# Optimization experiments

Hardware: AMD Instinct MI355X
Metric: run time of the kernel (lower is better)

Reference implementation:

```python
import jax, jax.numpy as jnp
import numpy as np

K_IN = 9      # input_patch_size
K_OUT = 3     # output_patch_size
C_IN = 4      # nb_of_input_features
C_OUT = 2     # nb_of_output_features
HID = 50      # int_layer_width
B, H, W = 16, 128, 128
CUT = K_IN // 2 - K_OUT // 2  # border pixels cut from output (3)


def _unfold(x, k):
    # x: [B, C, H, W] -> [B, C*k*k, L] with torch unfold ordering (c, ki, kj)
    b, c, h, w = x.shape
    ho, wo = h - k + 1, w - k + 1
    cols = jnp.stack([x[:, :, i:i + ho, j:j + wo]
                      for i in range(k) for j in range(k)], axis=2)  # [B,C,k*k,ho,wo]
    return cols.reshape(b, c * k * k, ho * wo)


def _fold_add(patches, oh, ow):
    # patches: [B, C, k, k, ho, wo] -> overlap-add into [B, C, oh, ow]
    b, c, k, _, ho, wo = patches.shape
    out = jnp.zeros((b, c, oh, ow), dtype=patches.dtype)
    for i in range(k):
        for j in range(k):
            out = out.at[:, :, i:i + ho, j:j + wo].add(patches[:, :, i, j])
    return out


def setup_inputs() -> dict:
    key = jax.random.key(0)
    ks = jax.random.split(key, 7)
    f_in = C_IN * K_IN * K_IN      # 324
    f_out = C_OUT * K_OUT * K_OUT  # 18
    s1 = 1.0 / np.sqrt(f_in)
    s2 = 1.0 / np.sqrt(HID)
    return {
        "x": jax.random.normal(ks[0], (B, C_IN, H, W), dtype=jnp.float32),
        "W1": jax.random.uniform(ks[1], (f_in, HID), jnp.float32, -s1, s1),
        "b1": jax.random.uniform(ks[2], (HID,), jnp.float32, -s1, s1),
        "W2": jax.random.uniform(ks[3], (HID, HID), jnp.float32, -s2, s2),
        "b2": jax.random.uniform(ks[4], (HID,), jnp.float32, -s2, s2),
        "W3": jax.random.uniform(ks[5], (HID, f_out), jnp.float32, -s2, s2),
        "b3": jax.random.uniform(ks[6], (f_out,), jnp.float32, -s2, s2),
    }


def reference(x, W1, b1, W2, b2, W3, b3):
    b, c, h, w = x.shape
    oh, ow = h - 2 * CUT, w - 2 * CUT          # 122, 122
    ho, wo = h - K_IN + 1, w - K_IN + 1        # 120, 120 (= oh-K_OUT+1)
    # unfold -> [B, L, C_in*K_in^2] -> flatten rows
    cols = _unfold(x, K_IN)                    # [B, 324, L]
    feats = cols.transpose(0, 2, 1).reshape(b * ho * wo, -1)
    # 3-layer MLP
    hmid = jax.nn.relu(feats @ W1 + b1)
    hmid = jax.nn.relu(hmid @ W2 + b2)
    out = hmid @ W3 + b3                       # [B*L, C_out*K_out^2]
    # fold (overlap-add), torch feature ordering (c, ki, kj)
    patches = out.reshape(b, ho, wo, C_OUT, K_OUT, K_OUT)
    patches = patches.transpose(0, 3, 4, 5, 1, 2)  # [B, C_out, k, k, ho, wo]
    res = _fold_add(patches, oh, ow)
    # divisor = fold(unfold(ones)) -> per-pixel overlap count
    ones_patches = jnp.ones((1, 1, K_OUT, K_OUT, ho, wo), dtype=x.dtype)
    divisor = _fold_add(ones_patches, oh, ow)  # [1,1,oh,ow]
    return res / divisor
```

## Files before the change

kernel.cpp:

```cpp
#include <hip/hip_runtime.h>
#include <hip/hip_bf16.h>

#define BATCH   16
#define C_INF   4
#define H_IN    128
#define W_IN    128
#define HID     50
#define F_OUT   18
#define HO      120
#define WO      120
#define OH      122
#define OW      122
#define NPOS    (BATCH * HO * WO)
#define MBLK    128
#define NBLKS   (NPOS / MBLK)

#define NB1     (11*4*2*64*8)
#define NB2     (2*4*2*64*8)
#define NB3     (2*2*2*64*8)
#define NWF     (NB1 + NB2 + NB3)
#define WOFF    (NPOS * F_OUT)

typedef float  v4f    __attribute__((ext_vector_type(4)));
typedef short  short4v __attribute__((ext_vector_type(4)));
typedef short  short8 __attribute__((ext_vector_type(8)));
typedef __bf16 v8bf   __attribute__((ext_vector_type(8)));
typedef int    v4i    __attribute__((ext_vector_type(4)));
typedef v4f    v4f_a4 __attribute__((aligned(4)));

__device__ inline short f2bf_hi(float x) {
    __hip_bfloat16 h = __float2bfloat16(x);
    return __builtin_bit_cast(short, h);
}
__device__ inline float bf2f(short s) {
    __hip_bfloat16 h = __builtin_bit_cast(__hip_bfloat16, s);
    return __bfloat162float(h);
}

__device__ inline int slot_to_k1(int s, int qb, int e) {
    if (s < 9) {
        int pair = s*4 + qb;
        int c = pair/9, ki = pair - c*9;
        return c*81 + ki*9 + e;
    }
    int r = (s-9)*32 + qb*8 + e;
    if (r >= 36) return -1;
    int c = r/9, ki = r - c*9;
    return c*81 + ki*9 + 8;
}

__global__ __launch_bounds__(256)
void prep_kernel(const float* __restrict__ W1, const float* __restrict__ W2,
                 const float* __restrict__ W3, short* __restrict__ wf)
{
    int i = blockIdx.x * 256 + threadIdx.x;
    if (i >= NWF) return;
    float val;
    int p;
    if (i < NB1) {
        int t = i;
        int e = t & 7, lane = (t >> 3) & 63; p = (t >> 9) & 1;
        int rest = t >> 10;
        int u = rest & 3, s = rest >> 2;
        int k = slot_to_k1(s, lane >> 4, e);
        int n = u*16 + (lane & 15);
        val = (k >= 0 && n < HID) ? W1[k*HID + n] : 0.f;
    } else if (i < NB1 + NB2) {
        int t = i - NB1;
        int e = t & 7, lane = (t >> 3) & 63; p = (t >> 9) & 1;
        int rest = t >> 10;
        int u = rest & 3, s = rest >> 2;
        int k = s*32 + ((lane >> 4) << 3) + e;
        int n = u*16 + (lane & 15);
        val = (k < HID && n < HID) ? W2[k*HID + n] : 0.f;
    } else {
        int t = i - NB1 - NB2;
        int e = t & 7, lane = (t >> 3) & 63; p = (t >> 9) & 1;
        int rest = t >> 10;
        int u = rest & 1, s = rest >> 1;
        int k = s*32 + ((lane >> 4) << 3) + e;
        int n = u*16 + (lane & 15);
        val = (k < HID && n < F_OUT) ? W3[k*F_OUT + n] : 0.f;
    }
    short hi = f2bf_hi(val);
    wf[i] = (p == 0) ? hi : f2bf_hi(val - bf2f(hi));
}

__global__ __launch_bounds__(256, 4)
void mfma_mlp(const float* __restrict__ x,
              const float* __restrict__ b1, const float* __restrict__ b2,
              const float* __restrict__ b3,
              const short* __restrict__ wf, short* __restrict__ out3)
{
    __shared__ short h_hi[128 * 72];

    const int tid  = threadIdx.x;
    const int lane = tid & 63;
    const int w    = tid >> 6;
    const int q    = lane >> 4, col = lane & 15;
    const int mbase = blockIdx.x * MBLK;
    const int mw    = w * 32;

    float bias1[4], bias2[4], bias3[2];
    #pragma unroll
    for (int u = 0; u < 4; ++u) {
        int j = u*16 + col;
        bias1[u] = (j < HID) ? b1[j] : 0.f;
        bias2[u] = (j < HID) ? b2[j] : 0.f;
    }
    #pragma unroll
    for (int u = 0; u < 2; ++u) {
        int j = u*16 + col;
        bias3[u] = (j < F_OUT) ? b3[j] : 0.f;
    }

    int xbase[2];
    #pragma unroll
    for (int t = 0; t < 2; ++t) {
        int pos = mbase + mw + t*16 + col;
        int b   = pos / (HO*WO); int rem = pos - b*(HO*WO);
        int y   = rem / WO;      int xc  = rem - y*WO;
        xbase[t] = b*(C_INF*H_IN*W_IN) + y*W_IN + xc;
    }

    const v4i* B1 = (const v4i*)wf;
    const v4i* B2 = (const v4i*)(wf + NB1);
    const v4i* B3 = (const v4i*)(wf + NB1 + NB2);

    v4f acc[2][4];
    #pragma unroll
    for (int t = 0; t < 2; ++t)
        #pragma unroll
        for (int u = 0; u < 4; ++u)
            acc[t][u] = (v4f){0.f, 0.f, 0.f, 0.f};

    #pragma unroll 3
    for (int s = 0; s < 9; ++s) {
        const int pair = s*4 + q;
        const int c = pair/9, ki = pair - c*9;
        const int off = c*(H_IN*W_IN) + ki*W_IN;

        v4i bhv[4], blv[4];
        #pragma unroll
        for (int u = 0; u < 4; ++u) {
            int fb = ((s*4 + u)*2)*64 + lane;
            bhv[u] = B1[fb];
            blv[u] = B1[fb + 64];
        }

        short8 ah[2];
        #pragma unroll
        for (int t = 0; t < 2; ++t) {
            const float* p = &x[xbase[t] + off];
            v4f fa  = *(const v4f_a4*)(p);
            v4f fb2 = *(const v4f_a4*)(p + 4);
            #pragma unroll
            for (int e = 0; e < 4; ++e) {
                ah[t][e]     = f2bf_hi(fa[e]);
                ah[t][e + 4] = f2bf_hi(fb2[e]);
            }
        }
        #pragma unroll
        for (int u = 0; u < 4; ++u) {
            v8bf bh = __builtin_bit_cast(v8bf, bhv[u]);
            v8bf bl = __builtin_bit_cast(v8bf, blv[u]);
            #pragma unroll
            for (int t = 0; t < 2; ++t) {
                v8bf a_h = __builtin_bit_cast(v8bf, ah[t]);
                acc[t][u] = __builtin_amdgcn_mfma_f32_16x16x32_bf16(a_h, bh, acc[t][u], 0, 0, 0);
                acc[t][u] = __builtin_amdgcn_mfma_f32_16x16x32_bf16(a_h, bl, acc[t][u], 0, 0, 0);
            }
        }
    }
    #pragma unroll
    for (int sr = 0; sr < 2; ++sr) {
        const int s = 9 + sr;
        short8 ah[2];
        #pragma unroll
        for (int e = 0; e < 8; ++e) {
            int r = sr*32 + q*8 + e;
            bool valid = (r < 36);
            int c = valid ? r/9 : 0;
            int ki = r - c*9;
            int off = c*(H_IN*W_IN) + ki*W_IN + 8;
            #pragma unroll
            for (int t = 0; t < 2; ++t) {
                float v = valid ? x[xbase[t] + off] : 0.f;
                ah[t][e] = f2bf_hi(v);
            }
        }
        #pragma unroll
        for (int u = 0; u < 4; ++u) {
            int fb = ((s*4 + u)*2)*64 + lane;
            v8bf bh = __builtin_bit_cast(v8bf, B1[fb]);
            v8bf bl = __builtin_bit_cast(v8bf, B1[fb + 64]);
            #pragma unroll
            for (int t = 0; t < 2; ++t) {
                v8bf a_h = __builtin_bit_cast(v8bf, ah[t]);
                acc[t][u] = __builtin_amdgcn_mfma_f32_16x16x32_bf16(a_h, bh, acc[t][u], 0, 0, 0);
                acc[t][u] = __builtin_amdgcn_mfma_f32_16x16x32_bf16(a_h, bl, acc[t][u], 0, 0, 0);
            }
        }
    }

    #pragma unroll
    for (int u = 0; u < 4; ++u) {
        #pragma unroll
        for (int t = 0; t < 2; ++t) {
            #pragma unroll
            for (int r = 0; r < 4; ++r) {
                float v = fmaxf(acc[t][u][r] + bias1[u], 0.f);
                int m = mw + t*16 + q*4 + r;
                h_hi[m*72 + u*16 + col] = f2bf_hi(v);
            }
        }
    }

    v4f acc2[2][4];
    #pragma unroll
    for (int t = 0; t < 2; ++t)
        #pragma unroll
        for (int u = 0; u < 4; ++u)
            acc2[t][u] = (v4f){0.f, 0.f, 0.f, 0.f};

    #pragma unroll
    for (int s = 0; s < 2; ++s) {
        short8 ah2[2];
        #pragma unroll
        for (int t = 0; t < 2; ++t) {
            int m = mw + t*16 + col;
            ah2[t] = *(const short8*)&h_hi[m*72 + s*32 + q*8];
        }
        #pragma unroll
        for (int u = 0; u < 4; ++u) {
            int fb = ((s*4 + u)*2)*64 + lane;
            v8bf bh = __builtin_bit_cast(v8bf, B2[fb]);
            v8bf bl = __builtin_bit_cast(v8bf, B2[fb + 64]);
            #pragma unroll
            for (int t = 0; t < 2; ++t) {
                v8bf a_h = __builtin_bit_cast(v8bf, ah2[t]);
                acc2[t][u] = __builtin_amdgcn_mfma_f32_16x16x32_bf16(a_h, bh, acc2[t][u], 0, 0, 0);
                acc2[t][u] = __builtin_amdgcn_mfma_f32_16x16x32_bf16(a_h, bl, acc2[t][u], 0, 0, 0);
            }
        }
    }

    #pragma unroll
    for (int u = 0; u < 4; ++u) {
        #pragma unroll
        for (int t = 0; t < 2; ++t) {
            #pragma unroll
            for (int r = 0; r < 4; ++r) {
                float v = fmaxf(acc2[t][u][r] + bias2[u], 0.f);
                int m = mw + t*16 + q*4 + r;
                h_hi[m*72 + u*16 + col] = f2bf_hi(v);
            }
        }
    }

    v4f acc3[2][2];
    #pragma unroll
    for (int t = 0; t < 2; ++t)
        #pragma unroll
        for (int u = 0; u < 2; ++u)
            acc3[t][u] = (v4f){0.f, 0.f, 0.f, 0.f};

    #pragma unroll
    for (int s = 0; s < 2; ++s) {
        short8 ah3[2];
        #pragma unroll
        for (int t = 0; t < 2; ++t) {
            int m = mw + t*16 + col;
            ah3[t] = *(const short8*)&h_hi[m*72 + s*32 + q*8];
        }
        #pragma unroll
        for (int u = 0; u < 2; ++u) {
            int fb = ((s*2 + u)*2)*64 + lane;
            v8bf bh = __builtin_bit_cast(v8bf, B3[fb]);
            v8bf bl = __builtin_bit_cast(v8bf, B3[fb + 64]);
            #pragma unroll
            for (int t = 0; t < 2; ++t) {
                v8bf a_h = __builtin_bit_cast(v8bf, ah3[t]);
                acc3[t][u] = __builtin_amdgcn_mfma_f32_16x16x32_bf16(a_h, bh, acc3[t][u], 0, 0, 0);
                acc3[t][u] = __builtin_amdgcn_mfma_f32_16x16x32_bf16(a_h, bl, acc3[t][u], 0, 0, 0);
            }
        }
    }

    #pragma unroll
    for (int u = 0; u < 2; ++u) {
        int j = u*16 + col;
        if (j < F_OUT) {
            #pragma unroll
            for (int t = 0; t < 2; ++t) {
                short4v vs;
                #pragma unroll
                for (int r = 0; r < 4; ++r) vs[r] = f2bf_hi(acc3[t][u][r] + bias3[u]);
                *(short4v*)&out3[j*NPOS + mbase + mw + t*16 + q*4] = vs;
            }
        }
    }
}

__global__ __launch_bounds__(256)
void fold_kernel(const short* __restrict__ out3, float* __restrict__ out)
{
    const int idx = blockIdx.x * 256 + threadIdx.x;
    const int total = BATCH * 2 * OH * OW;
    if (idx >= total) return;

    int t = idx;
    const int ox = t % OW; t /= OW;
    const int oy = t % OH; t /= OH;
    const int c  = t & 1;  t >>= 1;
    const int b  = t;

    const int ylo = max(0, oy - 2), yhi = min(HO - 1, oy);
    const int xlo = max(0, ox - 2), xhi = min(WO - 1, ox);

    float s = 0.f;
    for (int y = ylo; y <= yhi; ++y) {
        const int ki = oy - y;
        for (int xx = xlo; xx <= xhi; ++xx) {
            const int kj = ox - xx;
            const int o  = (c*3 + ki)*3 + kj;
            s += bf2f(out3[o*NPOS + (b*HO + y)*WO + xx]);
        }
    }
    const float div = (float)((yhi - ylo + 1) * (xhi - xlo + 1));
    out[idx] = s / div;
}

extern "C" void kernel_launch(void* const* d_in, const int* in_sizes, int n_in,
                              void* d_out, int out_size, void* d_ws, size_t ws_size,
                              hipStream_t stream)
{
    const float* x  = (const float*)d_in[0];
    const float* W1 = (const float*)d_in[1];
    const float* b1 = (const float*)d_in[2];
    const float* W2 = (const float*)d_in[3];
    const float* b2 = (const float*)d_in[4];
    const float* W3 = (const float*)d_in[5];
    const float* b3 = (const float*)d_in[6];

    short* out3 = (short*)d_ws;
    short* wf   = out3 + WOFF;

    prep_kernel<<<(NWF + 255) / 256, 256, 0, stream>>>(W1, W2, W3, wf);

    mfma_mlp<<<NBLKS, 256, 0, stream>>>(x, b1, b2, b3, wf, out3);

    const int total = BATCH * 2 * OH * OW;
    fold_kernel<<<(total + 255) / 256, 256, 0, stream>>>(out3, (float*)d_out);
}
```

Measured before the change: 117.4 us.

## Pre-convert input to bf16, give each wave 64 rows, add fold fast path

The prep kernel gains extra blocks that convert x to bf16 once, so the MLP kernel loads 16-byte bf16 vectors instead of converting fp32 gathers in every tile. The MLP kernel drops to 128 threads per block, and each wave handles 64 rows (4 M-tiles), which reuses each B1/B2/B3 weight fragment load across twice as many MFMAs. The fold kernel gets an unrolled interior fast path with a constant divisor of 9. In exchange, the larger per-wave accumulator set raises register pressure (launch bounds now 128,3), and the separate conversion pass adds one extra read and write of x.

```diff
diff --git a/kernel.cpp b/kernel.cpp
--- a/kernel.cpp
+++ b/kernel.cpp
@@ -20,13 +20,16 @@
 #define NB3     (2*2*2*64*8)
 #define NWF     (NB1 + NB2 + NB3)
 #define WOFF    (NPOS * F_OUT)
-
-typedef float  v4f    __attribute__((ext_vector_type(4)));
+#define NXC     (BATCH * C_INF * H_IN * W_IN)
+#define PREP_BLOCKS  ((NWF + 255) / 256)
+#define XCONV_BLOCKS (NXC / (256 * 8))
+
+typedef float  v4f     __attribute__((ext_vector_type(4)));
 typedef short  short4v __attribute__((ext_vector_type(4)));
-typedef short  short8 __attribute__((ext_vector_type(8)));
-typedef __bf16 v8bf   __attribute__((ext_vector_type(8)));
-typedef int    v4i    __attribute__((ext_vector_type(4)));
-typedef v4f    v4f_a4 __attribute__((aligned(4)));
+typedef short  short8  __attribute__((ext_vector_type(8)));
+typedef __bf16 v8bf    __attribute__((ext_vector_type(8)));
+typedef int    v4i     __attribute__((ext_vector_type(4)));
+typedef short8 short8_a2 __attribute__((aligned(2)));
 
 __device__ inline short f2bf_hi(float x) {
     __hip_bfloat16 h = __float2bfloat16(x);
@@ -50,10 +53,23 @@
 }
 
 __global__ __launch_bounds__(256)
-void prep_kernel(const float* __restrict__ W1, const float* __restrict__ W2,
-                 const float* __restrict__ W3, short* __restrict__ wf)
+void prep_kernel(const float* __restrict__ x,
+                 const float* __restrict__ W1, const float* __restrict__ W2,
+                 const float* __restrict__ W3, short* __restrict__ wf,
+                 short* __restrict__ xbf)
 {
-    int i = blockIdx.x * 256 + threadIdx.x;
+    const int blk = blockIdx.x;
+    if (blk >= PREP_BLOCKS) {
+        const int j = ((blk - PREP_BLOCKS)*256 + (int)threadIdx.x) * 8;
+        v4f a = *(const v4f*)&x[j];
+        v4f b = *(const v4f*)&x[j + 4];
+        short8 s;
+        #pragma unroll
+        for (int e = 0; e < 4; ++e) { s[e] = f2bf_hi(a[e]); s[e+4] = f2bf_hi(b[e]); }
+        *(short8*)&xbf[j] = s;
+        return;
+    }
+    int i = blk * 256 + threadIdx.x;
     if (i >= NWF) return;
     float val;
     int p;
@@ -86,8 +102,8 @@
     wf[i] = (p == 0) ? hi : f2bf_hi(val - bf2f(hi));
 }
 
-__global__ __launch_bounds__(256, 4)
-void mfma_mlp(const float* __restrict__ x,
+__global__ __launch_bounds__(128, 3)
+void mfma_mlp(const short* __restrict__ xbf,
               const float* __restrict__ b1, const float* __restrict__ b2,
               const float* __restrict__ b3,
               const short* __restrict__ wf, short* __restrict__ out3)
@@ -99,7 +115,7 @@
     const int w    = tid >> 6;
     const int q    = lane >> 4, col = lane & 15;
     const int mbase = blockIdx.x * MBLK;
-    const int mw    = w * 32;
+    const int mw    = w * 64;
 
     float bias1[4], bias2[4], bias3[2];
     #pragma unroll
@@ -114,9 +130,9 @@
         bias3[u] = (j < F_OUT) ? b3[j] : 0.f;
     }
 
-    int xbase[2];
-    #pragma unroll
-    for (int t = 0; t < 2; ++t) {
+    int xbase[4];
+    #pragma unroll
+    for (int t = 0; t < 4; ++t) {
         int pos = mbase + mw + t*16 + col;
         int b   = pos / (HO*WO); int rem = pos - b*(HO*WO);
         int y   = rem / WO;      int xc  = rem - y*WO;
@@ -127,9 +143,9 @@
     const v4i* B2 = (const v4i*)(wf + NB1);
     const v4i* B3 = (const v4i*)(wf + NB1 + NB2);
 
-    v4f acc[2][4];
-    #pragma unroll
-    for (int t = 0; t < 2; ++t)
+    v4f acc[4][4];
+    #pragma unroll
+    for (int t = 0; t < 4; ++t)
         #pragma unroll
         for (int u = 0; u < 4; ++u)
             acc[t][u] = (v4f){0.f, 0.f, 0.f, 0.f};
@@ -148,24 +164,17 @@
             blv[u] = B1[fb + 64];
         }
 
-        short8 ah[2];
-        #pragma unroll
-        for (int t = 0; t < 2; ++t) {
-            const float* p = &x[xbase[t] + off];
-            v4f fa  = *(const v4f_a4*)(p);
-            v4f fb2 = *(const v4f_a4*)(p + 4);
-            #pragma unroll
-            for (int e = 0; e < 4; ++e) {
-                ah[t][e]     = f2bf_hi(fa[e]);
-                ah[t][e + 4] = f2bf_hi(fb2[e]);
-            }
-        }
+        short8 ah[4];
+        #pragma unroll
+        for (int t = 0; t < 4; ++t)
+            ah[t] = *(const short8_a2*)&xbf[xbase[t] + off];
+
         #pragma unroll
         for (int u = 0; u < 4; ++u) {
             v8bf bh = __builtin_bit_cast(v8bf, bhv[u]);
             v8bf bl = __builtin_bit_cast(v8bf, blv[u]);
             #pragma unroll
-            for (int t = 0; t < 2; ++t) {
+            for (int t = 0; t < 4; ++t) {
                 v8bf a_h = __builtin_bit_cast(v8bf, ah[t]);
                 acc[t][u] = __builtin_amdgcn_mfma_f32_16x16x32_bf16(a_h, bh, acc[t][u], 0, 0, 0);
                 acc[t][u] = __builtin_amdgcn_mfma_f32_16x16x32_bf16(a_h, bl, acc[t][u], 0, 0, 0);
@@ -175,7 +184,7 @@
     #pragma unroll
     for (int sr = 0; sr < 2; ++sr) {
         const int s = 9 + sr;
-        short8 ah[2];
+        short8 ah[4];
         #pragma unroll
         for (int e = 0; e < 8; ++e) {
             int r = sr*32 + q*8 + e;
@@ -184,10 +193,8 @@
             int ki = r - c*9;
             int off = c*(H_IN*W_IN) + ki*W_IN + 8;
             #pragma unroll
-            for (int t = 0; t < 2; ++t) {
-                float v = valid ? x[xbase[t] + off] : 0.f;
-                ah[t][e] = f2bf_hi(v);
-            }
+            for (int t = 0; t < 4; ++t)
+                ah[t][e] = valid ? xbf[xbase[t] + off] : (short)0;
         }
         #pragma unroll
         for (int u = 0; u < 4; ++u) {
@@ -195,7 +202,7 @@
             v8bf bh = __builtin_bit_cast(v8bf, B1[fb]);
             v8bf bl = __builtin_bit_cast(v8bf, B1[fb + 64]);
             #pragma unroll
-            for (int t = 0; t < 2; ++t) {
+            for (int t = 0; t < 4; ++t) {
                 v8bf a_h = __builtin_bit_cast(v8bf, ah[t]);
                 acc[t][u] = __builtin_amdgcn_mfma_f32_16x16x32_bf16(a_h, bh, acc[t][u], 0, 0, 0);
                 acc[t][u] = __builtin_amdgcn_mfma_f32_16x16x32_bf16(a_h, bl, acc[t][u], 0, 0, 0);
@@ -206,7 +213,7 @@
     #pragma unroll
     for (int u = 0; u < 4; ++u) {
         #pragma unroll
-        for (int t = 0; t < 2; ++t) {
+        for (int t = 0; t < 4; ++t) {
             #pragma unroll
             for (int r = 0; r < 4; ++r) {
                 float v = fmaxf(acc[t][u][r] + bias1[u], 0.f);
@@ -216,18 +223,18 @@
         }
     }
 
-    v4f acc2[2][4];
-    #pragma unroll
-    for (int t = 0; t < 2; ++t)
+    v4f acc2[4][4];
+    #pragma unroll
+    for (int t = 0; t < 4; ++t)
         #pragma unroll
         for (int u = 0; u < 4; ++u)
             acc2[t][u] = (v4f){0.f, 0.f, 0.f, 0.f};
 
     #pragma unroll
     for (int s = 0; s < 2; ++s) {
-        short8 ah2[2];
-        #pragma unroll
-        for (int t = 0; t < 2; ++t) {
+        short8 ah2[4];
+        #pragma unroll
+        for (int t = 0; t < 4; ++t) {
             int m = mw + t*16 + col;
             ah2[t] = *(const short8*)&h_hi[m*72 + s*32 + q*8];
         }
@@ -237,7 +244,7 @@
             v8bf bh = __builtin_bit_cast(v8bf, B2[fb]);
             v8bf bl = __builtin_bit_cast(v8bf, B2[fb + 64]);
             #pragma unroll
-            for (int t = 0; t < 2; ++t) {
+            for (int t = 0; t < 4; ++t) {
                 v8bf a_h = __builtin_bit_cast(v8bf, ah2[t]);
                 acc2[t][u] = __builtin_amdgcn_mfma_f32_16x16x32_bf16(a_h, bh, acc2[t][u], 0, 0, 0);
                 acc2[t][u] = __builtin_amdgcn_mfma_f32_16x16x32_bf16(a_h, bl, acc2[t][u], 0, 0, 0);
@@ -248,7 +255,7 @@
     #pragma unroll
     for (int u = 0; u < 4; ++u) {
         #pragma unroll
-        for (int t = 0; t < 2; ++t) {
+        for (int t = 0; t < 4; ++t) {
             #pragma unroll
             for (int r = 0; r < 4; ++r) {
                 float v = fmaxf(acc2[t][u][r] + bias2[u], 0.f);
@@ -258,18 +265,18 @@
         }
     }
 
-    v4f acc3[2][2];
-    #pragma unroll
-    for (int t = 0; t < 2; ++t)
+    v4f acc3[4][2];
+    #pragma unroll
+    for (int t = 0; t < 4; ++t)
         #pragma unroll
         for (int u = 0; u < 2; ++u)
             acc3[t][u] = (v4f){0.f, 0.f, 0.f, 0.f};
 
     #pragma unroll
     for (int s = 0; s < 2; ++s) {
-        short8 ah3[2];
-        #pragma unroll
-        for (int t = 0; t < 2; ++t) {
+        short8 ah3[4];
+        #pragma unroll
+        for (int t = 0; t < 4; ++t) {
             int m = mw + t*16 + col;
             ah3[t] = *(const short8*)&h_hi[m*72 + s*32 + q*8];
         }
@@ -279,7 +286,7 @@
             v8bf bh = __builtin_bit_cast(v8bf, B3[fb]);
             v8bf bl = __builtin_bit_cast(v8bf, B3[fb + 64]);
             #pragma unroll
-            for (int t = 0; t < 2; ++t) {
+            for (int t = 0; t < 4; ++t) {
                 v8bf a_h = __builtin_bit_cast(v8bf, ah3[t]);
                 acc3[t][u] = __builtin_amdgcn_mfma_f32_16x16x32_bf16(a_h, bh, acc3[t][u], 0, 0, 0);
                 acc3[t][u] = __builtin_amdgcn_mfma_f32_16x16x32_bf16(a_h, bl, acc3[t][u], 0, 0, 0);
@@ -292,7 +299,7 @@
         int j = u*16 + col;
         if (j < F_OUT) {
             #pragma unroll
-            for (int t = 0; t < 2; ++t) {
+            for (int t = 0; t < 4; ++t) {
                 short4v vs;
                 #pragma unroll
                 for (int r = 0; r < 4; ++r) vs[r] = f2bf_hi(acc3[t][u][r] + bias3[u]);
@@ -314,6 +321,23 @@
     const int oy = t % OH; t /= OH;
     const int c  = t & 1;  t >>= 1;
     const int b  = t;
+
+    if (oy >= 2 && oy < HO && ox >= 2 && ox < WO) {
+        const int base = (b*HO + (oy - 2))*WO + (ox - 2);
+        float s = 0.f;
+        #pragma unroll
+        for (int dy = 0; dy < 3; ++dy) {
+            const int ki = 2 - dy;
+            #pragma unroll
+            for (int dx = 0; dx < 3; ++dx) {
+                const int kj = 2 - dx;
+                const int o  = (c*3 + ki)*3 + kj;
+                s += bf2f(out3[o*NPOS + base + dy*WO + dx]);
+            }
+        }
+        out[idx] = s / 9.f;
+        return;
+    }
 
     const int ylo = max(0, oy - 2), yhi = min(HO - 1, oy);
     const int xlo = max(0, ox - 2), xhi = min(WO - 1, ox);
@@ -345,10 +369,11 @@
 
     short* out3 = (short*)d_ws;
     short* wf   = out3 + WOFF;
-
-    prep_kernel<<<(NWF + 255) / 256, 256, 0, stream>>>(W1, W2, W3, wf);
-
-    mfma_mlp<<<NBLKS, 256, 0, stream>>>(x, b1, b2, b3, wf, out3);
+    short* xbf  = wf + NWF;
+
+    prep_kernel<<<PREP_BLOCKS + XCONV_BLOCKS, 256, 0, stream>>>(x, W1, W2, W3, wf, xbf);
+
+    mfma_mlp<<<NBLKS, 128, 0, stream>>>(xbf, b1, b2, b3, wf, out3);
 
     const int total = BATCH * 2 * OH * OW;
     fold_kernel<<<(total + 255) / 256, 256, 0, stream>>>(out3, (float*)d_out);
```

After: 123.7 us. +5.4%, slower.

## Pre-convert input to bf16 even/odd copies, prefetch weights, vectorize fold

Applied to the files above, without the earlier changes.

Adds a pass in the prep kernel that converts x to bf16 twice, once as-is and once shifted by one element, so that every 8-element patch row can be loaded as one aligned short8. This removes the per-use fp32 to bf16 conversion and halves the bytes read in the MLP kernel. Layer-1 weight fragments are now double-buffered in registers, and launch bounds drop to 3 waves per SIMD to leave room for the extra registers. The fold kernel now handles 8 output pixels per thread with vector loads on interior tiles. The trade-offs are an extra 2x bf16 copy of x in the workspace, lower occupancy, and more code paths.

```diff
diff --git a/kernel.cpp b/kernel.cpp
--- a/kernel.cpp
+++ b/kernel.cpp
@@ -20,13 +20,17 @@
 #define NB3     (2*2*2*64*8)
 #define NWF     (NB1 + NB2 + NB3)
 #define WOFF    (NPOS * F_OUT)
-
-typedef float  v4f    __attribute__((ext_vector_type(4)));
+#define NXC     (BATCH * C_INF * H_IN * W_IN)
+#define PREP_BLOCKS  ((NWF + 255) / 256)
+#define XCONV_BLOCKS (NXC / (256 * 8))
+#define CW      16
+
+typedef float  v4f     __attribute__((ext_vector_type(4)));
 typedef short  short4v __attribute__((ext_vector_type(4)));
-typedef short  short8 __attribute__((ext_vector_type(8)));
-typedef __bf16 v8bf   __attribute__((ext_vector_type(8)));
-typedef int    v4i    __attribute__((ext_vector_type(4)));
-typedef v4f    v4f_a4 __attribute__((aligned(4)));
+typedef short  short8  __attribute__((ext_vector_type(8)));
+typedef __bf16 v8bf    __attribute__((ext_vector_type(8)));
+typedef int    v4i     __attribute__((ext_vector_type(4)));
+typedef short8 short8_a4 __attribute__((aligned(4)));
 
 __device__ inline short f2bf_hi(float x) {
     __hip_bfloat16 h = __float2bfloat16(x);
@@ -50,10 +54,29 @@
 }
 
 __global__ __launch_bounds__(256)
-void prep_kernel(const float* __restrict__ W1, const float* __restrict__ W2,
-                 const float* __restrict__ W3, short* __restrict__ wf)
+void prep_kernel(const float* __restrict__ x,
+                 const float* __restrict__ W1, const float* __restrict__ W2,
+                 const float* __restrict__ W3, short* __restrict__ wf,
+                 short* __restrict__ xe, short* __restrict__ xo)
 {
-    int i = blockIdx.x * 256 + threadIdx.x;
+    const int blk = blockIdx.x;
+    if (blk >= PREP_BLOCKS) {
+        const int j = ((blk - PREP_BLOCKS)*256 + (int)threadIdx.x) * 8;
+        v4f a = *(const v4f*)&x[j];
+        v4f b = *(const v4f*)&x[j + 4];
+        float c9 = (j + 8 < NXC) ? x[j + 8] : 0.f;
+        short s[9];
+        #pragma unroll
+        for (int e = 0; e < 4; ++e) { s[e] = f2bf_hi(a[e]); s[e+4] = f2bf_hi(b[e]); }
+        s[8] = f2bf_hi(c9);
+        short8 ve, vo;
+        #pragma unroll
+        for (int e = 0; e < 8; ++e) { ve[e] = s[e]; vo[e] = s[e+1]; }
+        *(short8*)&xe[j] = ve;
+        *(short8*)&xo[j] = vo;
+        return;
+    }
+    int i = blk * 256 + threadIdx.x;
     if (i >= NWF) return;
     float val;
     int p;
@@ -86,8 +109,8 @@
     wf[i] = (p == 0) ? hi : f2bf_hi(val - bf2f(hi));
 }
 
-__global__ __launch_bounds__(256, 4)
-void mfma_mlp(const float* __restrict__ x,
+__global__ __launch_bounds__(256, 3)
+void mfma_mlp(const short* __restrict__ xe, const short* __restrict__ xo,
               const float* __restrict__ b1, const float* __restrict__ b2,
               const float* __restrict__ b3,
               const short* __restrict__ wf, short* __restrict__ out3)
@@ -114,18 +137,19 @@
         bias3[u] = (j < F_OUT) ? b3[j] : 0.f;
     }
 
-    int xbase[2];
+    const short* xp[2];
     #pragma unroll
     for (int t = 0; t < 2; ++t) {
         int pos = mbase + mw + t*16 + col;
         int b   = pos / (HO*WO); int rem = pos - b*(HO*WO);
         int y   = rem / WO;      int xc  = rem - y*WO;
-        xbase[t] = b*(C_INF*H_IN*W_IN) + y*W_IN + xc;
-    }
-
-    const v4i* B1 = (const v4i*)wf;
-    const v4i* B2 = (const v4i*)(wf + NB1);
-    const v4i* B3 = (const v4i*)(wf + NB1 + NB2);
+        int bi  = b*(C_INF*H_IN*W_IN) + y*W_IN + xc;
+        xp[t] = (bi & 1) ? (xo + (bi - 1)) : (xe + bi);
+    }
+
+    const v4i* B1L = (const v4i*)wf + lane;
+    const v4i* B2L = (const v4i*)(wf + NB1) + lane;
+    const v4i* B3L = (const v4i*)(wf + NB1 + NB2) + lane;
 
     v4f acc[2][4];
     #pragma unroll
@@ -134,47 +158,47 @@
         for (int u = 0; u < 4; ++u)
             acc[t][u] = (v4f){0.f, 0.f, 0.f, 0.f};
 
-    #pragma unroll 3
+    v4i bh[2][4], bl[2][4];
+    #pragma unroll
+    for (int u = 0; u < 4; ++u) { bh[0][u] = B1L[u*128]; bl[0][u] = B1L[u*128 + 64]; }
+
+    #pragma unroll
     for (int s = 0; s < 9; ++s) {
+        const int cur = s & 1, nxt = cur ^ 1;
+        #pragma unroll
+        for (int u = 0; u < 4; ++u) {
+            bh[nxt][u] = B1L[((s+1)*4 + u)*128];
+            bl[nxt][u] = B1L[((s+1)*4 + u)*128 + 64];
+        }
         const int pair = s*4 + q;
         const int c = pair/9, ki = pair - c*9;
         const int off = c*(H_IN*W_IN) + ki*W_IN;
-
-        v4i bhv[4], blv[4];
+        short8 ah[2];
+        #pragma unroll
+        for (int t = 0; t < 2; ++t)
+            ah[t] = *(const short8_a4*)(xp[t] + off);
         #pragma unroll
         for (int u = 0; u < 4; ++u) {
-            int fb = ((s*4 + u)*2)*64 + lane;
-            bhv[u] = B1[fb];
-            blv[u] = B1[fb + 64];
-        }
-
-        short8 ah[2];
-        #pragma unroll
-        for (int t = 0; t < 2; ++t) {
-            const float* p = &x[xbase[t] + off];
-            v4f fa  = *(const v4f_a4*)(p);
-            v4f fb2 = *(const v4f_a4*)(p + 4);
-            #pragma unroll
-            for (int e = 0; e < 4; ++e) {
-                ah[t][e]     = f2bf_hi(fa[e]);
-                ah[t][e + 4] = f2bf_hi(fb2[e]);
-            }
-        }
-        #pragma unroll
-        for (int u = 0; u < 4; ++u) {
-            v8bf bh = __builtin_bit_cast(v8bf, bhv[u]);
-            v8bf bl = __builtin_bit_cast(v8bf, blv[u]);
+            v8bf bhc = __builtin_bit_cast(v8bf, bh[cur][u]);
+            v8bf blc = __builtin_bit_cast(v8bf, bl[cur][u]);
             #pragma unroll
             for (int t = 0; t < 2; ++t) {
                 v8bf a_h = __builtin_bit_cast(v8bf, ah[t]);
-                acc[t][u] = __builtin_amdgcn_mfma_f32_16x16x32_bf16(a_h, bh, acc[t][u], 0, 0, 0);
-                acc[t][u] = __builtin_amdgcn_mfma_f32_16x16x32_bf16(a_h, bl, acc[t][u], 0, 0, 0);
+                acc[t][u] = __builtin_amdgcn_mfma_f32_16x16x32_bf16(a_h, bhc, acc[t][u], 0, 0, 0);
+                acc[t][u] = __builtin_amdgcn_mfma_f32_16x16x32_bf16(a_h, blc, acc[t][u], 0, 0, 0);
             }
         }
     }
     #pragma unroll
     for (int sr = 0; sr < 2; ++sr) {
-        const int s = 9 + sr;
+        const int cur = (9 + sr) & 1, nxt = cur ^ 1;
+        if (sr == 0) {
+            #pragma unroll
+            for (int u = 0; u < 4; ++u) {
+                bh[nxt][u] = B1L[(10*4 + u)*128];
+                bl[nxt][u] = B1L[(10*4 + u)*128 + 64];
+            }
+        }
         short8 ah[2];
         #pragma unroll
         for (int e = 0; e < 8; ++e) {
@@ -184,21 +208,18 @@
             int ki = r - c*9;
             int off = c*(H_IN*W_IN) + ki*W_IN + 8;
             #pragma unroll
-            for (int t = 0; t < 2; ++t) {
-                float v = valid ? x[xbase[t] + off] : 0.f;
-                ah[t][e] = f2bf_hi(v);
-            }
+            for (int t = 0; t < 2; ++t)
+                ah[t][e] = valid ? xp[t][off] : (short)0;
         }
         #pragma unroll
         for (int u = 0; u < 4; ++u) {
-            int fb = ((s*4 + u)*2)*64 + lane;
-            v8bf bh = __builtin_bit_cast(v8bf, B1[fb]);
-            v8bf bl = __builtin_bit_cast(v8bf, B1[fb + 64]);
+            v8bf bhc = __builtin_bit_cast(v8bf, bh[cur][u]);
+            v8bf blc = __builtin_bit_cast(v8bf, bl[cur][u]);
             #pragma unroll
             for (int t = 0; t < 2; ++t) {
                 v8bf a_h = __builtin_bit_cast(v8bf, ah[t]);
-                acc[t][u] = __builtin_amdgcn_mfma_f32_16x16x32_bf16(a_h, bh, acc[t][u], 0, 0, 0);
-                acc[t][u] = __builtin_amdgcn_mfma_f32_16x16x32_bf16(a_h, bl, acc[t][u], 0, 0, 0);
+                acc[t][u] = __builtin_amdgcn_mfma_f32_16x16x32_bf16(a_h, bhc, acc[t][u], 0, 0, 0);
+                acc[t][u] = __builtin_amdgcn_mfma_f32_16x16x32_bf16(a_h, blc, acc[t][u], 0, 0, 0);
             }
         }
     }
@@ -233,14 +254,13 @@
         }
         #pragma unroll
         for (int u = 0; u < 4; ++u) {
-            int fb = ((s*4 + u)*2)*64 + lane;
-            v8bf bh = __builtin_bit_cast(v8bf, B2[fb]);
-            v8bf bl = __builtin_bit_cast(v8bf, B2[fb + 64]);
+            v8bf bhc = __builtin_bit_cast(v8bf, B2L[(s*4 + u)*128]);
+            v8bf blc = __builtin_bit_cast(v8bf, B2L[(s*4 + u)*128 + 64]);
             #pragma unroll
             for (int t = 0; t < 2; ++t) {
                 v8bf a_h = __builtin_bit_cast(v8bf, ah2[t]);
-                acc2[t][u] = __builtin_amdgcn_mfma_f32_16x16x32_bf16(a_h, bh, acc2[t][u], 0, 0, 0);
-                acc2[t][u] = __builtin_amdgcn_mfma_f32_16x16x32_bf16(a_h, bl, acc2[t][u], 0, 0, 0);
+                acc2[t][u] = __builtin_amdgcn_mfma_f32_16x16x32_bf16(a_h, bhc, acc2[t][u], 0, 0, 0);
+                acc2[t][u] = __builtin_amdgcn_mfma_f32_16x16x32_bf16(a_h, blc, acc2[t][u], 0, 0, 0);
             }
         }
     }
@@ -275,14 +295,13 @@
         }
         #pragma unroll
         for (int u = 0; u < 2; ++u) {
-            int fb = ((s*2 + u)*2)*64 + lane;
-            v8bf bh = __builtin_bit_cast(v8bf, B3[fb]);
-            v8bf bl = __builtin_bit_cast(v8bf, B3[fb + 64]);
+            v8bf bhc = __builtin_bit_cast(v8bf, B3L[(s*2 + u)*128]);
+            v8bf blc = __builtin_bit_cast(v8bf, B3L[(s*2 + u)*128 + 64]);
             #pragma unroll
             for (int t = 0; t < 2; ++t) {
                 v8bf a_h = __builtin_bit_cast(v8bf, ah3[t]);
-                acc3[t][u] = __builtin_amdgcn_mfma_f32_16x16x32_bf16(a_h, bh, acc3[t][u], 0, 0, 0);
-                acc3[t][u] = __builtin_amdgcn_mfma_f32_16x16x32_bf16(a_h, bl, acc3[t][u], 0, 0, 0);
+                acc3[t][u] = __builtin_amdgcn_mfma_f32_16x16x32_bf16(a_h, bhc, acc3[t][u], 0, 0, 0);
+                acc3[t][u] = __builtin_amdgcn_mfma_f32_16x16x32_bf16(a_h, blc, acc3[t][u], 0, 0, 0);
             }
         }
     }
@@ -306,29 +325,60 @@
 void fold_kernel(const short* __restrict__ out3, float* __restrict__ out)
 {
     const int idx = blockIdx.x * 256 + threadIdx.x;
-    const int total = BATCH * 2 * OH * OW;
+    const int total = BATCH * 2 * OH * CW;
     if (idx >= total) return;
 
     int t = idx;
-    const int ox = t % OW; t /= OW;
+    const int cx = t % CW; t /= CW;
     const int oy = t % OH; t /= OH;
     const int c  = t & 1;  t >>= 1;
     const int b  = t;
-
-    const int ylo = max(0, oy - 2), yhi = min(HO - 1, oy);
-    const int xlo = max(0, ox - 2), xhi = min(WO - 1, ox);
-
-    float s = 0.f;
-    for (int y = ylo; y <= yhi; ++y) {
-        const int ki = oy - y;
-        for (int xx = xlo; xx <= xhi; ++xx) {
-            const int kj = ox - xx;
-            const int o  = (c*3 + ki)*3 + kj;
-            s += bf2f(out3[o*NPOS + (b*HO + y)*WO + xx]);
-        }
-    }
-    const float div = (float)((yhi - ylo + 1) * (xhi - xlo + 1));
-    out[idx] = s / div;
+    const int ox0 = cx * 8;
+
+    if (oy >= 2 && oy < HO && cx >= 1 && cx <= 14) {
+        float accv[8];
+        #pragma unroll
+        for (int e = 0; e < 8; ++e) accv[e] = 0.f;
+        #pragma unroll
+        for (int ki = 0; ki < 3; ++ki) {
+            const int y    = oy - ki;
+            const int rowb = (b*HO + y)*WO;
+            const int ob   = (c*3 + ki)*3;
+            short8 v0 = *(const short8_a4*)&out3[(ob + 0)*NPOS + rowb + ox0];
+            short8 v1 = *(const short8_a4*)&out3[(ob + 1)*NPOS + rowb + ox0 - 2];
+            int   v1b = *(const int*)      &out3[(ob + 1)*NPOS + rowb + ox0 + 6];
+            short8 v2 = *(const short8_a4*)&out3[(ob + 2)*NPOS + rowb + ox0 - 2];
+            #pragma unroll
+            for (int e = 0; e < 8; ++e) {
+                accv[e] += bf2f(v0[e]);
+                accv[e] += (e < 7) ? bf2f(v1[e + 1]) : bf2f((short)(v1b & 0xffff));
+                accv[e] += bf2f(v2[e]);
+            }
+        }
+        float* op = &out[((b*2 + c)*OH + oy)*OW + ox0];
+        #pragma unroll
+        for (int e = 0; e < 8; ++e) op[e] = accv[e] / 9.f;
+        return;
+    }
+
+    #pragma unroll
+    for (int e = 0; e < 8; ++e) {
+        const int ox = ox0 + e;
+        if (ox >= OW) break;
+        const int ylo = max(0, oy - 2), yhi = min(HO - 1, oy);
+        const int xlo = max(0, ox - 2), xhi = min(WO - 1, ox);
+        float s = 0.f;
+        for (int y = ylo; y <= yhi; ++y) {
+            const int ki = oy - y;
+            for (int xx = xlo; xx <= xhi; ++xx) {
+                const int kj = ox - xx;
+                const int o  = (c*3 + ki)*3 + kj;
+                s += bf2f(out3[o*NPOS + (b*HO + y)*WO + xx]);
+            }
+        }
+        const float div = (float)((yhi - ylo + 1) * (xhi - xlo + 1));
+        out[((b*2 + c)*OH + oy)*OW + ox] = s / div;
+    }
 }
 
 extern "C" void kernel_launch(void* const* d_in, const int* in_sizes, int n_in,
@@ -345,11 +395,13 @@
 
     short* out3 = (short*)d_ws;
     short* wf   = out3 + WOFF;
-
-    prep_kernel<<<(NWF + 255) / 256, 256, 0, stream>>>(W1, W2, W3, wf);
-
-    mfma_mlp<<<NBLKS, 256, 0, stream>>>(x, b1, b2, b3, wf, out3);
-
-    const int total = BATCH * 2 * OH * OW;
+    short* xe   = wf + NWF;
+    short* xo   = xe + NXC;
+
+    prep_kernel<<<PREP_BLOCKS + XCONV_BLOCKS, 256, 0, stream>>>(x, W1, W2, W3, wf, xe, xo);
+
+    mfma_mlp<<<NBLKS, 256, 0, stream>>>(xe, xo, b1, b2, b3, wf, out3);
+
+    const int total = BATCH * 2 * OH * CW;
     fold_kernel<<<(total + 255) / 256, 256, 0, stream>>>(out3, (float*)d_out);
 }
```

After: 133.7 us. 1.14x slower.
